# Kernel tuning notes

Hardware: AMD Instinct MI355X
Metric: run time of the kernel (lower is better)

The kernel has to match this reference:

```python
import jax, jax.numpy as jnp
import numpy as np

DEPTH, DIM, HEADS, DH, MLP, N, B = 6, 192, 12, 16, 768, 256, 32
INNER = HEADS * DH  # 192


def setup_inputs() -> dict:
    key = jax.random.key(0)
    ks = jax.random.split(key, 10)
    w = lambda i, shape: jax.random.normal(ks[i], shape, dtype=jnp.float32) * 0.02
    return {
        'x': jax.random.normal(ks[0], (B, N, DIM), dtype=jnp.float32),
        'ln1_g': jnp.ones((DEPTH, DIM), jnp.float32),
        'ln1_b': jnp.zeros((DEPTH, DIM), jnp.float32),
        'Wq': w(1, (DEPTH, DIM, INNER)),
        'Wkv': w(2, (DEPTH, DIM, 2 * INNER)),
        'lsa_scale': jnp.full((DEPTH, HEADS), DH ** -0.5, dtype=jnp.float32),
        'mix_pre': jax.random.normal(ks[3], (DEPTH, HEADS, HEADS), dtype=jnp.float32),
        'mix_post': jax.random.normal(ks[4], (DEPTH, HEADS, HEADS), dtype=jnp.float32),
        'Wo': w(5, (DEPTH, INNER, DIM)),
        'bo': jnp.zeros((DEPTH, DIM), jnp.float32),
        'ls1': jnp.full((DEPTH, DIM), 0.1, dtype=jnp.float32),
        'ln2_g': jnp.ones((DEPTH, DIM), jnp.float32),
        'ln2_b': jnp.zeros((DEPTH, DIM), jnp.float32),
        'W1': w(6, (DEPTH, DIM, MLP)),
        'b1': jnp.zeros((DEPTH, MLP), jnp.float32),
        'W2': w(7, (DEPTH, MLP, DIM)),
        'b2': jnp.zeros((DEPTH, DIM), jnp.float32),
        'ls2': jnp.full((DEPTH, DIM), 0.1, dtype=jnp.float32),
    }


def _ln(x, g, b, eps=1e-5):
    m = x.mean(-1, keepdims=True)
    v = ((x - m) ** 2).mean(-1, keepdims=True)
    return (x - m) * jax.lax.rsqrt(v + eps) * g + b


def _heads(t, b, n):
    # (b, n, h*d) -> (b, h, n, d)
    return t.reshape(b, n, HEADS, DH).transpose(0, 2, 1, 3)


def _forward(x, ln1_g, ln1_b, Wq, Wkv, lsa_scale, mix_pre, mix_post, Wo, bo,
             ls1, ln2_g, ln2_b, W1, b1, W2, b2, ls2):
    b, n, _ = x.shape
    diag = jnp.arange(n)
    for l in range(DEPTH):
        # --- PreNorm + talking-heads LSA attention + LayerScale(0.1) ---
        h = _ln(x, ln1_g[l], ln1_b[l])
        q = _heads(h @ Wq[l], b, n)
        k, v = jnp.split(h @ Wkv[l], 2, axis=-1)
        k, v = _heads(k, b, n), _heads(v, b, n)
        dots = jnp.einsum('bhid,bhjd->bhij', q, k) * lsa_scale[l][None, :, None, None]
        # LSA: source sets diagonal to -1e-09 (literal, near-zero) when if_patch_attn
        dots = dots.at[:, :, diag, diag].set(-1e-9)
        dots = jnp.einsum('bhij,hg->bgij', dots, mix_pre[l])
        a = jax.nn.softmax(dots, axis=-1)
        a = jnp.einsum('bhij,hg->bgij', a, mix_post[l])
        o = jnp.einsum('bhij,bhjd->bhid', a, v)
        o = o.transpose(0, 2, 1, 3).reshape(b, n, INNER) @ Wo[l] + bo[l]
        x = x + o * ls1[l]
        # --- PreNorm + GELU FFN + LayerScale(0.1) ---
        h2 = _ln(x, ln2_g[l], ln2_b[l])
        f = jax.nn.gelu(h2 @ W1[l] + b1[l], approximate=False) @ W2[l] + b2[l]
        x = x + f * ls2[l]
    return x


def reference(x, ln1_g, ln1_b, Wq, Wkv, lsa_scale, mix_pre, mix_post, Wo, bo,
              ls1, ln2_g, ln2_b, W1, b1, W2, b2, ls2):
    return _forward(x, ln1_g, ln1_b, Wq, Wkv, lsa_scale, mix_pre, mix_post, Wo,
                    bo, ls1, ln2_g, ln2_b, W1, b1, W2, b2, ls2)
```

## Files before the change

### kernel.cpp

```cpp
#include <hip/hip_runtime.h>
#include <hip/hip_bf16.h>

#define DEPTH   6
#define DIM     192
#define HEADS   12
#define DH      16
#define MLPD    768
#define SEQ     256
#define BATCH   32
#define ROWS    (BATCH*SEQ)

typedef __attribute__((ext_vector_type(8))) short short8;
typedef __attribute__((ext_vector_type(4))) float f32x4;
typedef __attribute__((ext_vector_type(4))) _Float16 half4;
typedef __attribute__((ext_vector_type(8))) _Float16 half8;
typedef __hip_bfloat16 bf16_t;
typedef _Float16 f16_t;

__device__ __forceinline__ bf16_t f2b(float v){ return __float2bfloat16(v); }
__device__ __forceinline__ ushort f2u(float v){
    union{ bf16_t b; ushort u; } w; w.b = __float2bfloat16(v); return w.u;
}
__device__ __forceinline__ f16_t u2h(ushort u){ union{ ushort u; f16_t h; } w; w.u = u; return w.h; }
__device__ __forceinline__ ushort h2u(f16_t h){ union{ ushort u; f16_t h; } w; w.h = h; return w.u; }

__device__ __forceinline__ void async16(ushort* lds, const ushort* gp){
    __builtin_amdgcn_global_load_lds(
        (const __attribute__((address_space(1))) uint*)gp,
        (__attribute__((address_space(3))) uint*)lds, 16, 0, 0);
}

__global__ void copy_kernel(const float* __restrict__ x, float* __restrict__ xr, int n){
    int i = blockIdx.x*256 + threadIdx.x;
    if (i < n) xr[i] = x[i];
}

__device__ __forceinline__ void wt_tile(const float* __restrict__ W,
        ushort* __restrict__ WT, int K, int N, int l, int tx, int ty,
        int tid, ushort* T){
    const float* src = W + ((size_t)l*K + tx*64)*N + ty*64;
    ushort* dst = WT + ((size_t)l*N + ty*64)*K + tx*64;
    int r = tid >> 2, c4 = (tid & 3)*16;
    #pragma unroll
    for (int u=0; u<4; u++){
        float4 v = *(const float4*)(src + (size_t)r*N + c4 + u*4);
        T[(c4+u*4+0)*72 + r] = f2u(v.x);
        T[(c4+u*4+1)*72 + r] = f2u(v.y);
        T[(c4+u*4+2)*72 + r] = f2u(v.z);
        T[(c4+u*4+3)*72 + r] = f2u(v.w);
    }
    __syncthreads();
    int n = tid >> 2, k8 = (tid & 3)*16;
    #pragma unroll
    for (int u=0; u<2; u++)
        *(uint4*)(dst + (size_t)n*K + k8 + u*8) = *(uint4*)&T[n*72 + k8 + u*8];
}

__global__ __launch_bounds__(256) void wt_all(
        const float* __restrict__ Wq, const float* __restrict__ Wkv,
        const float* __restrict__ Wo, const float* __restrict__ W1,
        const float* __restrict__ W2,
        ushort* __restrict__ WqT, ushort* __restrict__ WkvT,
        ushort* __restrict__ WoT, ushort* __restrict__ W1T,
        ushort* __restrict__ W2T){
    __shared__ ushort T[64*72];
    int id = blockIdx.x, l = blockIdx.y, tid = threadIdx.x;
    if (id < 9)       wt_tile(Wq,  WqT,  192, 192, l, id/3,       id%3,       tid, T);
    else if (id < 27) wt_tile(Wkv, WkvT, 192, 384, l, (id-9)/6,   (id-9)%6,   tid, T);
    else if (id < 36) wt_tile(Wo,  WoT,  192, 192, l, (id-27)/3,  (id-27)%3,  tid, T);
    else if (id < 72) wt_tile(W1,  W1T,  192, 768, l, (id-36)/12, (id-36)%12, tid, T);
    else              wt_tile(W2,  W2T,  768, 192, l, (id-72)/3,  (id-72)%3,  tid, T);
}

__global__ __launch_bounds__(256) void ln_kernel(
        const float* __restrict__ xres, const float* __restrict__ ln_g,
        const float* __restrict__ ln_b, ushort* __restrict__ out){
    int lane = threadIdx.x & 63, w = threadIdx.x >> 6;
    int row = blockIdx.x*4 + w;
    const float* xr = xres + (size_t)row*DIM;
    float v0 = xr[lane], v1 = xr[lane+64], v2 = xr[lane+128];
    float s = v0+v1+v2;
    #pragma unroll
    for (int off=32; off; off>>=1) s += __shfl_xor(s, off, 64);
    float m = s*(1.0f/192.0f);
    float d0=v0-m, d1=v1-m, d2=v2-m;
    float q = d0*d0+d1*d1+d2*d2;
    #pragma unroll
    for (int off=32; off; off>>=1) q += __shfl_xor(q, off, 64);
    float inv = rsqrtf(q*(1.0f/192.0f) + 1e-5f);
    float g0 = ln_g[lane], g1 = ln_g[lane+64], g2 = ln_g[lane+128];
    float e0 = ln_b[lane], e1 = ln_b[lane+64], e2 = ln_b[lane+128];
    ushort* dst = out + (size_t)row*DIM;
    dst[lane]     = f2u(d0*inv*g0 + e0);
    dst[lane+64]  = f2u(d1*inv*g1 + e1);
    dst[lane+128] = f2u(d2*inv*g2 + e2);
}

template<int MODE>
__global__ __launch_bounds__(256) void gemm_ln_kernel(
        const ushort* __restrict__ Aln, const ushort* __restrict__ BT0,
        const ushort* __restrict__ BT1, const float* __restrict__ bias,
        f16_t* __restrict__ out0, f16_t* __restrict__ out1){
    __shared__ ushort As[6*2048];
    __shared__ ushort Bs[6*2048];
    int tid = threadIdx.x, lane = tid & 63, w = tid >> 6;
    int bm = blockIdx.x*64;
    int bn = blockIdx.y*64;
    {
        const ushort* ap = Aln + (size_t)(bm + (tid>>2))*DIM + (tid&3)*8;
        const ushort* bt; int bnl;
        if (MODE == 0 && bn >= DIM){ bt = BT1; bnl = bn - DIM; }
        else { bt = BT0; bnl = bn; }
        const ushort* bp = bt + (size_t)(bnl + (tid>>2))*DIM + (tid&3)*8;
        #pragma unroll
        for (int c=0; c<6; c++){
            async16(&As[c*2048 + tid*8], ap + c*32);
            async16(&Bs[c*2048 + tid*8], bp + c*32);
        }
    }
    __syncthreads();
    int wrow = w >> 1, wcol = w & 1;
    int quad = lane >> 4, mr = lane & 15;
    f32x4 acc[2][2] = {};
    #pragma unroll
    for (int c = 0; c < 6; c++){
        short8 a0 = *(const short8*)&As[c*2048 + (wrow*32+mr)*32    + quad*8];
        short8 a1 = *(const short8*)&As[c*2048 + (wrow*32+16+mr)*32 + quad*8];
        short8 b0 = *(const short8*)&Bs[c*2048 + (wcol*32+mr)*32    + quad*8];
        short8 b1 = *(const short8*)&Bs[c*2048 + (wcol*32+16+mr)*32 + quad*8];
        acc[0][0] = __builtin_amdgcn_mfma_f32_16x16x32_bf16(a0, b0, acc[0][0], 0,0,0);
        acc[0][1] = __builtin_amdgcn_mfma_f32_16x16x32_bf16(a0, b1, acc[0][1], 0,0,0);
        acc[1][0] = __builtin_amdgcn_mfma_f32_16x16x32_bf16(a1, b0, acc[1][0], 0,0,0);
        acc[1][1] = __builtin_amdgcn_mfma_f32_16x16x32_bf16(a1, b1, acc[1][1], 0,0,0);
    }
    #pragma unroll
    for (int rr=0; rr<2; rr++){
        #pragma unroll
        for (int cc=0; cc<2; cc++){
            int col = bn + wcol*32 + cc*16 + mr;
            if (MODE == 0){
                f16_t* op; size_t st;
                if (col < DIM){ op = out0 + col; st = DIM; }
                else          { op = out1 + (col - DIM); st = 2*DIM; }
                #pragma unroll
                for (int tt=0; tt<4; tt++){
                    int row = bm + wrow*32 + rr*16 + quad*4 + tt;
                    op[(size_t)row*st] = (f16_t)acc[rr][cc][tt];
                }
            } else {
                float bv = bias[col];
                #pragma unroll
                for (int tt=0; tt<4; tt++){
                    int row = bm + wrow*32 + rr*16 + quad*4 + tt;
                    float z = acc[rr][cc][tt] + bv;
                    ((bf16_t*)out0)[(size_t)row*MLPD + col] =
                        f2b(0.5f*z*(1.0f + erff(z*0.70710678118654752f)));
                }
            }
        }
    }
}

template<int ROUNDS>
__global__ __launch_bounds__(256) void gemm_a_kernel(
        const ushort* __restrict__ A, const ushort* __restrict__ BT,
        const float* __restrict__ bias, const float* __restrict__ ls,
        float* __restrict__ xres){
    const int K = ROUNDS*192;
    __shared__ ushort As[6*2048];
    __shared__ ushort Bs[6*2048];
    int tid = threadIdx.x, lane = tid & 63, w = tid >> 6;
    int wrow = w >> 1, wcol = w & 1;
    int bm = blockIdx.x*64, bn = blockIdx.y*64;
    int quad = lane >> 4, mr = lane & 15;
    const ushort* ap = A  + (size_t)(bm + (tid>>2))*K + (tid&3)*8;
    const ushort* bp = BT + (size_t)(bn + (tid>>2))*K + (tid&3)*8;
    f32x4 acc[2][2] = {};
    for (int r = 0; r < ROUNDS; r++){
        #pragma unroll
        for (int c=0; c<6; c++){
            async16(&As[c*2048 + tid*8], ap + r*192 + c*32);
            async16(&Bs[c*2048 + tid*8], bp + r*192 + c*32);
        }
        __syncthreads();
        #pragma unroll
        for (int c=0; c<6; c++){
            short8 a0 = *(const short8*)&As[c*2048 + (wrow*32+mr)*32    + quad*8];
            short8 a1 = *(const short8*)&As[c*2048 + (wrow*32+16+mr)*32 + quad*8];
            short8 b0 = *(const short8*)&Bs[c*2048 + (wcol*32+mr)*32    + quad*8];
            short8 b1 = *(const short8*)&Bs[c*2048 + (wcol*32+16+mr)*32 + quad*8];
            acc[0][0] = __builtin_amdgcn_mfma_f32_16x16x32_bf16(a0, b0, acc[0][0], 0,0,0);
            acc[0][1] = __builtin_amdgcn_mfma_f32_16x16x32_bf16(a0, b1, acc[0][1], 0,0,0);
            acc[1][0] = __builtin_amdgcn_mfma_f32_16x16x32_bf16(a1, b0, acc[1][0], 0,0,0);
            acc[1][1] = __builtin_amdgcn_mfma_f32_16x16x32_bf16(a1, b1, acc[1][1], 0,0,0);
        }
        if (r+1 < ROUNDS) __syncthreads();
    }
    #pragma unroll
    for (int rr=0; rr<2; rr++){
        #pragma unroll
        for (int cc=0; cc<2; cc++){
            int col = bn + wcol*32 + cc*16 + mr;
            float bv = bias[col], lv = ls[col];
            #pragma unroll
            for (int tt=0; tt<4; tt++){
                int row = bm + wrow*32 + rr*16 + quad*4 + tt;
                xres[(size_t)row*DIM + col] += (acc[rr][cc][tt] + bv)*lv;
            }
        }
    }
}

#define SLAB    4488
#define IST     280
#define KV_OFF  53856
#define ROWP    200
#define Q_OFF   66656
#define POST_OFF 70112
#define PRE_OFF 71776
#define LTOT    71920

__global__ __launch_bounds__(1024, 1) void attn_kernel(
        const f16_t* __restrict__ qb, const f16_t* __restrict__ kvb,
        const float* __restrict__ lsa, const float* __restrict__ pre,
        const float* __restrict__ post, const ushort* __restrict__ WoT,
        const float* __restrict__ bo, const float* __restrict__ ls1,
        float* __restrict__ xres){
    __shared__ ushort L[LTOT];
    int tid  = threadIdx.x;
    int lane = tid & 63, w = tid >> 6;
    int quad = lane >> 4, nr = lane & 15;
    int b  = blockIdx.x >> 4;
    int i0 = (blockIdx.x & 15) << 4;

    {
        uint* Z = (uint*)&L[KV_OFF];
        for (int k = tid; k < (LTOT - KV_OFF)/2; k += 1024) Z[k] = 0;
    }
    __syncthreads();

    if (tid < 384){
        int e = tid*8, i = e/DIM, d = e%DIM, hh = d >> 4;
        float sc = lsa[hh];
        union { uint4 v; f16_t h[8]; } iv, ov;
        iv.v = *(const uint4*)(qb + (size_t)(b*SEQ + i0 + i)*DIM + d);
        #pragma unroll
        for (int u=0; u<8; u++) ov.h[u] = (f16_t)((float)iv.h[u]*sc);
        *(uint4*)&L[Q_OFF + i*ROWP + d] = ov.v;
    } else if (tid < 512){
        for (int k = tid-384; k < 256; k += 128){
            int gg = k >> 4, hh = k & 15;
            if (gg < 12 && hh < 12)
                L[POST_OFF + k] = h2u((f16_t)post[hh*12+gg]);
        }
    } else if (tid < 640){
        for (int k = tid-512; k < 144; k += 128)
            L[PRE_OFF + k] = h2u((f16_t)pre[k]);
    }
    auto stage_kv = [&](int c, int coloff){
        for (int u = tid; u < 1536; u += 1024){
            int e = u*8;
            int j = e/DIM, d = e%DIM;
            uint4 v = *(const uint4*)(kvb + (size_t)(b*SEQ + c*64 + j)*(2*DIM) + coloff + d);
            *(uint4*)&L[KV_OFF + j*ROWP + d] = v;
        }
    };
    __syncthreads();

    half4 postTf = *(const half4*)&L[POST_OFF + nr*16 + quad*4];

    {
        int jg = w*16 + nr;
        const f16_t* krow = kvb + (size_t)(b*SEQ + jg)*(2*DIM);
        half8 qh[6], kh[6];
        #pragma unroll
        for (int c=0; c<6; c++){
            union{ short8 s; half8 h; } a, k2;
            a.s  = *(const short8*)&L[Q_OFF + nr*ROWP + c*32 + quad*8];
            k2.s = *(const short8*)(const void*)(krow + c*32 + quad*8);
            qh[c] = a.h; kh[c] = k2.h;
        }
        int dd = jg - (i0 + quad*4);
        int hb = (quad>>1)*12;
        #pragma unroll
        for (int g=0; g<12; g++){
            f32x4 a = {0,0,0,0};
            #pragma unroll
            for (int c=0; c<6; c++){
                f16_t s = u2h(L[PRE_OFF + hb + c*24 + g]);
                a = __builtin_amdgcn_mfma_f32_16x16x32_f16(qh[c]*s, kh[c], a, 0,0,0);
            }
            ushort* sp = &L[g*SLAB + jg];
            sp[(quad*4+0)*IST] = (dd==0) ? (ushort)0 : h2u((f16_t)a[0]);
            sp[(quad*4+1)*IST] = (dd==1) ? (ushort)0 : h2u((f16_t)a[1]);
            sp[(quad*4+2)*IST] = (dd==2) ? (ushort)0 : h2u((f16_t)a[2]);
            sp[(quad*4+3)*IST] = (dd==3) ? (ushort)0 : h2u((f16_t)a[3]);
        }
    }
    __syncthreads();

    for (int r = w; r < 192; r += 16){
        int g = r >> 4, i = r & 15;
        ushort* sp = &L[g*SLAB + i*IST];
        ushort4 uv = *(ushort4*)&sp[lane*4];
        float e0 = __expf((float)u2h(uv.x));
        float e1 = __expf((float)u2h(uv.y));
        float e2 = __expf((float)u2h(uv.z));
        float e3 = __expf((float)u2h(uv.w));
        float ssum = e0+e1+e2+e3;
        #pragma unroll
        for (int off=32; off; off>>=1) ssum += __shfl_xor(ssum, off, 64);
        float rin = 1.0f/ssum;
        uv.x = h2u((f16_t)(e0*rin)); uv.y = h2u((f16_t)(e1*rin));
        uv.z = h2u((f16_t)(e2*rin)); uv.w = h2u((f16_t)(e3*rin));
        *(ushort4*)&sp[lane*4] = uv;
    }
    __syncthreads();

    for (int s = 0; s < 16; s++){
        int cb = s*16 + w;
        int i = cb >> 4, jb = cb & 15;
        int colbase = i*IST + jb*16 + nr;
        half4 bv;
        #pragma unroll
        for (int t=0; t<4; t++) bv[t] = u2h(L[(quad*4+t)*SLAB + colbase]);
        f32x4 cc = __builtin_amdgcn_mfma_f32_16x16x16f16(postTf, bv, (f32x4){0,0,0,0}, 0,0,0);
        if (quad < 3){
            #pragma unroll
            for (int t=0; t<4; t++) L[(quad*4+t)*SLAB + colbase] = h2u((f16_t)cc[t]);
        }
    }
    __syncthreads();

    f32x4 oacc = {0,0,0,0};
    for (int c = 0; c < 4; c++){
        stage_kv(c, DIM);
        __syncthreads();
        if (w < 12){
            int g = w;
            #pragma unroll
            for (int ks = 0; ks < 4; ks++){
                int jl = ks*16 + quad*4;
                half4 av = *(const half4*)&L[g*SLAB + nr*IST + c*64 + jl];
                half4 bv;
                #pragma unroll
                for (int t=0; t<4; t++) bv[t] = u2h(L[KV_OFF + (jl+t)*ROWP + g*16 + nr]);
                oacc = __builtin_amdgcn_mfma_f32_16x16x16f16(av, bv, oacc, 0,0,0);
            }
        }
        __syncthreads();
    }

    if (w < 12){
        int g = w;
        #pragma unroll
        for (int t=0; t<4; t++){
            int i = quad*4 + t;
            L[Q_OFF + i*ROWP + g*16 + nr] = f2u(oacc[t]);
        }
    }
    __syncthreads();

    if (w < 12){
        f32x4 wacc = {0,0,0,0};
        int ct = w;
        const ushort* wg = WoT + (size_t)(ct*16 + nr)*192;
        #pragma unroll
        for (int c = 0; c < 3; c++){
            #pragma unroll
            for (int sub = 0; sub < 2; sub++){
                int k0 = c*64 + sub*32;
                short8 av = *(const short8*)&L[Q_OFF + nr*ROWP + k0 + quad*8];
                short8 bv = *(const short8*)(wg + k0 + quad*8);
                wacc = __builtin_amdgcn_mfma_f32_16x16x32_bf16(av, bv, wacc, 0,0,0);
            }
        }
        int col = ct*16 + nr;
        float bv2 = bo[col], lv = ls1[col];
        #pragma unroll
        for (int t=0; t<4; t++){
            int row = b*SEQ + i0 + quad*4 + t;
            xres[(size_t)row*DIM + col] += (wacc[t] + bv2)*lv;
        }
    }
}

extern "C" void kernel_launch(void* const* d_in, const int* in_sizes, int n_in,
                              void* d_out, int out_size, void* d_ws, size_t ws_size,
                              hipStream_t stream){
    const float* x    = (const float*)d_in[0];
    const float* ln1g = (const float*)d_in[1];
    const float* ln1b = (const float*)d_in[2];
    const float* Wq   = (const float*)d_in[3];
    const float* Wkv  = (const float*)d_in[4];
    const float* lsa  = (const float*)d_in[5];
    const float* pre  = (const float*)d_in[6];
    const float* post = (const float*)d_in[7];
    const float* Wo   = (const float*)d_in[8];
    const float* bo   = (const float*)d_in[9];
    const float* ls1  = (const float*)d_in[10];
    const float* ln2g = (const float*)d_in[11];
    const float* ln2b = (const float*)d_in[12];
    const float* W1   = (const float*)d_in[13];
    const float* b1   = (const float*)d_in[14];
    const float* W2   = (const float*)d_in[15];
    const float* b2   = (const float*)d_in[16];
    const float* ls2  = (const float*)d_in[17];
    float* xres = (float*)d_out;

    char* ws = (char*)d_ws;
    f16_t*  qb  = (f16_t*)ws;
    f16_t*  kvb = (f16_t*)(ws + (size_t)ROWS*DIM*2);
    bf16_t* fb  = (bf16_t*)ws;
    char* p = ws + (size_t)ROWS*MLPD*2;
    ushort* WqT  = (ushort*)p; p += (size_t)DEPTH*DIM*DIM*2;
    ushort* WkvT = (ushort*)p; p += (size_t)DEPTH*DIM*2*DIM*2;
    ushort* WoT  = (ushort*)p; p += (size_t)DEPTH*DIM*DIM*2;
    ushort* W1T  = (ushort*)p; p += (size_t)DEPTH*DIM*MLPD*2;
    ushort* W2T  = (ushort*)p; p += (size_t)DEPTH*MLPD*DIM*2;
    ushort* lnb  = (ushort*)p; p += (size_t)ROWS*DIM*2;

    int ntot = ROWS*DIM;
    copy_kernel<<<ntot/256, 256, 0, stream>>>(x, xres, ntot);
    wt_all<<<dim3(108, 6), 256, 0, stream>>>(Wq, Wkv, Wo, W1, W2,
                                             WqT, WkvT, WoT, W1T, W2T);
    for (int l = 0; l < DEPTH; l++){
        ln_kernel<<<ROWS/4, 256, 0, stream>>>(xres, ln1g + l*DIM, ln1b + l*DIM, lnb);
        gemm_ln_kernel<0><<<dim3(128,9), 256, 0, stream>>>(lnb,
                WqT + (size_t)l*DIM*DIM, WkvT + (size_t)l*DIM*2*DIM,
                nullptr, qb, kvb);
        attn_kernel<<<BATCH*(SEQ/16), 1024, 0, stream>>>(qb, kvb, lsa + l*HEADS,
                pre + l*HEADS*HEADS, post + l*HEADS*HEADS,
                WoT + (size_t)l*DIM*DIM, bo + l*DIM, ls1 + l*DIM, xres);
        ln_kernel<<<ROWS/4, 256, 0, stream>>>(xres, ln2g + l*DIM, ln2b + l*DIM, lnb);
        gemm_ln_kernel<1><<<dim3(128,12), 256, 0, stream>>>(lnb,
                W1T + (size_t)l*DIM*MLPD, nullptr, b1 + l*MLPD, (f16_t*)fb, nullptr);
        gemm_a_kernel<4><<<dim3(128,3), 256, 0, stream>>>((const ushort*)fb,
                W2T + (size_t)l*MLPD*DIM, b2 + l*DIM, ls2 + l*DIM, xres);
    }
}
```

Before: 619.4 us.

## Store V transposed from QKV GEMM so attention reads V with vector loads

The QKV GEMM epilogue now writes K to its own row-major buffer and V in a transposed per-batch layout (batch, dim, seq) as packed half4 stores. The attention kernel then stages V tiles into LDS with the sequence index contiguous. The PV MFMA operand becomes a single half4 LDS load instead of four strided scalar reads. This cuts LDS traffic and bank conflicts in the PV loop, at the cost of a different global write pattern in the GEMM epilogue and a revised LDS layout.

```diff
diff --git a/kernel.cpp b/kernel.cpp
--- a/kernel.cpp
+++ b/kernel.cpp
@@ -100,7 +100,8 @@
 __global__ __launch_bounds__(256) void gemm_ln_kernel(
         const ushort* __restrict__ Aln, const ushort* __restrict__ BT0,
         const ushort* __restrict__ BT1, const float* __restrict__ bias,
-        f16_t* __restrict__ out0, f16_t* __restrict__ out1){
+        f16_t* __restrict__ out0, f16_t* __restrict__ out1,
+        f16_t* __restrict__ out2){
     __shared__ ushort As[6*2048];
     __shared__ ushort Bs[6*2048];
     int tid = threadIdx.x, lane = tid & 63, w = tid >> 6;
@@ -139,13 +140,21 @@
         for (int cc=0; cc<2; cc++){
             int col = bn + wcol*32 + cc*16 + mr;
             if (MODE == 0){
-                f16_t* op; size_t st;
-                if (col < DIM){ op = out0 + col; st = DIM; }
-                else          { op = out1 + (col - DIM); st = 2*DIM; }
-                #pragma unroll
-                for (int tt=0; tt<4; tt++){
-                    int row = bm + wrow*32 + rr*16 + quad*4 + tt;
-                    op[(size_t)row*st] = (f16_t)acc[rr][cc][tt];
+                if (col < 2*DIM){
+                    f16_t* op = (col < DIM) ? (out0 + col) : (out1 + col - DIM);
+                    #pragma unroll
+                    for (int tt=0; tt<4; tt++){
+                        int row = bm + wrow*32 + rr*16 + quad*4 + tt;
+                        op[(size_t)row*DIM] = (f16_t)acc[rr][cc][tt];
+                    }
+                } else {
+                    int d = col - 2*DIM;
+                    int row0 = bm + wrow*32 + rr*16 + quad*4;
+                    int bb = row0 >> 8, j0 = row0 & 255;
+                    half4 pk;
+                    #pragma unroll
+                    for (int tt=0; tt<4; tt++) pk[tt] = (f16_t)acc[rr][cc][tt];
+                    *(half4*)(out2 + (((size_t)(bb*DIM + d)) << 8) + j0) = pk;
                 }
             } else {
                 float bv = bias[col];
@@ -214,14 +223,16 @@
 #define SLAB    4488
 #define IST     280
 #define KV_OFF  53856
+#define VJP     72
 #define ROWP    200
-#define Q_OFF   66656
-#define POST_OFF 70112
-#define PRE_OFF 71776
-#define LTOT    71920
+#define Q_OFF   67680
+#define POST_OFF 70880
+#define PRE_OFF 71136
+#define LTOT    71808
 
 __global__ __launch_bounds__(1024, 1) void attn_kernel(
-        const f16_t* __restrict__ qb, const f16_t* __restrict__ kvb,
+        const f16_t* __restrict__ qb, const f16_t* __restrict__ kb,
+        const f16_t* __restrict__ vTg,
         const float* __restrict__ lsa, const float* __restrict__ pre,
         const float* __restrict__ post, const ushort* __restrict__ WoT,
         const float* __restrict__ bo, const float* __restrict__ ls1,
@@ -257,12 +268,12 @@
         for (int k = tid-512; k < 144; k += 128)
             L[PRE_OFF + k] = h2u((f16_t)pre[k]);
     }
-    auto stage_kv = [&](int c, int coloff){
+    auto stage_v = [&](int c){
         for (int u = tid; u < 1536; u += 1024){
             int e = u*8;
-            int j = e/DIM, d = e%DIM;
-            uint4 v = *(const uint4*)(kvb + (size_t)(b*SEQ + c*64 + j)*(2*DIM) + coloff + d);
-            *(uint4*)&L[KV_OFF + j*ROWP + d] = v;
+            int d = e >> 6, j = e & 63;
+            uint4 v = *(const uint4*)(vTg + (((size_t)(b*DIM + d)) << 8) + c*64 + j);
+            *(uint4*)&L[KV_OFF + d*VJP + j] = v;
         }
     };
     __syncthreads();
@@ -271,7 +282,7 @@
 
     {
         int jg = w*16 + nr;
-        const f16_t* krow = kvb + (size_t)(b*SEQ + jg)*(2*DIM);
+        const f16_t* krow = kb + (size_t)(b*SEQ + jg)*DIM;
         half8 qh[6], kh[6];
         #pragma unroll
         for (int c=0; c<6; c++){
@@ -334,7 +345,7 @@
 
     f32x4 oacc = {0,0,0,0};
     for (int c = 0; c < 4; c++){
-        stage_kv(c, DIM);
+        stage_v(c);
         __syncthreads();
         if (w < 12){
             int g = w;
@@ -342,9 +353,7 @@
             for (int ks = 0; ks < 4; ks++){
                 int jl = ks*16 + quad*4;
                 half4 av = *(const half4*)&L[g*SLAB + nr*IST + c*64 + jl];
-                half4 bv;
-                #pragma unroll
-                for (int t=0; t<4; t++) bv[t] = u2h(L[KV_OFF + (jl+t)*ROWP + g*16 + nr]);
+                half4 bv = *(const half4*)&L[KV_OFF + (g*16 + nr)*VJP + jl];
                 oacc = __builtin_amdgcn_mfma_f32_16x16x16f16(av, bv, oacc, 0,0,0);
             }
         }
@@ -410,7 +419,8 @@
 
     char* ws = (char*)d_ws;
     f16_t*  qb  = (f16_t*)ws;
-    f16_t*  kvb = (f16_t*)(ws + (size_t)ROWS*DIM*2);
+    f16_t*  kb  = (f16_t*)(ws + (size_t)ROWS*DIM*2);
+    f16_t*  vT  = (f16_t*)(ws + (size_t)ROWS*DIM*4);
     bf16_t* fb  = (bf16_t*)ws;
     char* p = ws + (size_t)ROWS*MLPD*2;
     ushort* WqT  = (ushort*)p; p += (size_t)DEPTH*DIM*DIM*2;
@@ -428,13 +438,14 @@
         ln_kernel<<<ROWS/4, 256, 0, stream>>>(xres, ln1g + l*DIM, ln1b + l*DIM, lnb);
         gemm_ln_kernel<0><<<dim3(128,9), 256, 0, stream>>>(lnb,
                 WqT + (size_t)l*DIM*DIM, WkvT + (size_t)l*DIM*2*DIM,
-                nullptr, qb, kvb);
-        attn_kernel<<<BATCH*(SEQ/16), 1024, 0, stream>>>(qb, kvb, lsa + l*HEADS,
-                pre + l*HEADS*HEADS, post + l*HEADS*HEADS,
+                nullptr, qb, kb, vT);
+        attn_kernel<<<BATCH*(SEQ/16), 1024, 0, stream>>>(qb, kb, vT,
+                lsa + l*HEADS, pre + l*HEADS*HEADS, post + l*HEADS*HEADS,
                 WoT + (size_t)l*DIM*DIM, bo + l*DIM, ls1 + l*DIM, xres);
         ln_kernel<<<ROWS/4, 256, 0, stream>>>(xres, ln2g + l*DIM, ln2b + l*DIM, lnb);
         gemm_ln_kernel<1><<<dim3(128,12), 256, 0, stream>>>(lnb,
-                W1T + (size_t)l*DIM*MLPD, nullptr, b1 + l*MLPD, (f16_t*)fb, nullptr);
+                W1T + (size_t)l*DIM*MLPD, nullptr, b1 + l*MLPD, (f16_t*)fb, nullptr,
+                nullptr);
         gemm_a_kernel<4><<<dim3(128,3), 256, 0, stream>>>((const ushort*)fb,
                 W2T + (size_t)l*MLPD*DIM, b2 + l*DIM, ls2 + l*DIM, xres);
     }
```

Result: no change. 615.2 us (-0.7%).
